# Performance work log

Measured on AMD Instinct MI355X. Metric: run time of the kernel, lower is better.

## Reference

```python
import jax, jax.numpy as jnp
import numpy as np

K = 4       # wavelet basis size
C = 4       # wavelet channels
ALPHA = 64  # retained Fourier modes per SparseKernelFT
L = 0       # coarsest-level cutoff


def setup_inputs() -> dict:
    key = jax.random.key(0)
    ks = jax.random.split(key, 14)
    B, N = 32, 16384
    ck = C * K
    wscale = 1.0 / (ck * ck)  # matches torch.rand(...)/in_ch^2 scale

    def cw(k1, k2):
        return (jax.random.normal(k1, (ck, ck, ALPHA), jnp.float32) * wscale,
                jax.random.normal(k2, (ck, ck, ALPHA), jnp.float32) * wscale)

    wA_re, wA_im = cw(ks[1], ks[2])
    wB_re, wB_im = cw(ks[3], ks[4])
    wC_re, wC_im = cw(ks[5], ks[6])
    fs = 1.0 / np.sqrt(2.0 * K)  # stand-in scale for orthonormal Legendre filter banks
    return {
        "x": jax.random.normal(ks[0], (B, N, C, K), jnp.float32),
        "ec_s": jax.random.normal(ks[7], (2 * K, K), jnp.float32) * fs,
        "ec_d": jax.random.normal(ks[8], (2 * K, K), jnp.float32) * fs,
        "rc_e": jax.random.normal(ks[9], (2 * K, K), jnp.float32) * fs,
        "rc_o": jax.random.normal(ks[10], (2 * K, K), jnp.float32) * fs,
        "t0_w": jax.random.normal(ks[11], (K, K), jnp.float32) / np.sqrt(K),
        "t0_b": jnp.zeros((K,), jnp.float32),
        "wA_re": wA_re, "wA_im": wA_im,
        "wB_re": wB_re, "wB_im": wB_im,
        "wC_re": wC_re, "wC_im": wC_im,
    }


def _sparse_ft(x, w_re, w_im):
    # SparseKernelFT (1D): rfft -> truncated-mode complex mixing -> irfft.
    B, N, c, k = x.shape
    ck = c * k
    xr = x.reshape(B, N, ck).transpose(0, 2, 1)        # (B, ck, N)
    xf = jnp.fft.rfft(xr)                               # (B, ck, N//2+1)
    nf = N // 2 + 1
    l = min(ALPHA, nf)
    w = (w_re + 1j * w_im)[:, :, :l]                    # (ck, ck, l) complex
    out = jnp.einsum('bix,iox->box', xf[:, :, :l], w)
    out_full = jnp.zeros((B, ck, nf), dtype=out.dtype).at[:, :, :l].set(out)
    y = jnp.fft.irfft(out_full, n=N)                    # real (B, ck, N)
    return y.transpose(0, 2, 1).reshape(B, N, c, k)


def _forward(x, ec_s, ec_d, rc_e, rc_o, t0_w, t0_b,
             wA_re, wA_im, wB_re, wB_im, wC_re, wC_im):
    B, N, c, k = x.shape
    ns = int(np.log2(N))
    Ud, Us = [], []
    # decomposition: N -> N/2 -> ... -> 2^L
    for _ in range(ns - L):
        xa = jnp.concatenate([x[:, ::2], x[:, 1::2]], axis=-1)  # (B, n/2, c, 2k)
        d = xa @ ec_d   # detail coefficients
        x = xa @ ec_s   # scale coefficients
        Ud.append(_sparse_ft(d, wA_re, wA_im) + _sparse_ft(x, wB_re, wB_im))
        Us.append(_sparse_ft(d, wC_re, wC_im))
    # coarsest-scale linear map T0 over last dim k
    x = x @ t0_w.T + t0_b
    # reconstruction with even/odd interleaving
    for i in range(ns - 1 - L, -1, -1):
        x = x + Us[i]
        xc = jnp.concatenate([x, Ud[i]], axis=-1)   # (B, n, c, 2k)
        x_e = xc @ rc_e                              # (B, n, c, k)
        x_o = xc @ rc_o
        b, n = x_e.shape[0], x_e.shape[1]
        x = jnp.stack([x_e, x_o], axis=2).reshape(b, 2 * n, c, k)
    return x


def reference(x, ec_s, ec_d, rc_e, rc_o, t0_w, t0_b,
              wA_re, wA_im, wB_re, wB_im, wC_re, wC_im):
    return _forward(x, ec_s, ec_d, rc_e, rc_o, t0_w, t0_b,
                    wA_re, wA_im, wB_re, wB_im, wC_re, wC_im)
```

## Files before the change

### kernel.cpp

```cpp
#include <hip/hip_runtime.h>

#define TWO_PI 6.28318530717958647692f

constexpr int BB   = 32;
constexpr int NTOT = 16384;
constexpr int CKd  = 16;
constexpr int NLEV = 14;

__device__ __forceinline__ void decomp_row(const float* __restrict__ src,
                                           const float* __restrict__ ec_s,
                                           const float* __restrict__ ec_d,
                                           float* d, float* s)
{
  float xa[32];
#pragma unroll
  for (int q = 0; q < 8; ++q) {
    float4 v = reinterpret_cast<const float4*>(src)[q];
    xa[q*4+0] = v.x; xa[q*4+1] = v.y; xa[q*4+2] = v.z; xa[q*4+3] = v.w;
  }
#pragma unroll
  for (int c = 0; c < 4; ++c) {
#pragma unroll
    for (int j = 0; j < 4; ++j) {
      float ad = 0.f, as = 0.f;
#pragma unroll
      for (int m = 0; m < 4; ++m) {
        const float xe = xa[c*4+m];
        const float xo = xa[16+c*4+m];
        ad += xe * ec_d[m*4+j] + xo * ec_d[(4+m)*4+j];
        as += xe * ec_s[m*4+j] + xo * ec_s[(4+m)*4+j];
      }
      d[c*4+j] = ad; s[c*4+j] = as;
    }
  }
}

__global__ __launch_bounds__(256) void fwd_big(
    const float* __restrict__ xin, float* __restrict__ xout,
    float* __restrict__ Fd, float* __restrict__ Fx,
    const float* __restrict__ ec_s, const float* __restrict__ ec_d,
    int nhalf)
{
  __shared__ float smem[16384];
  float* Pd = smem;
  float* Md = smem + 4096;
  float* Ps = smem + 8192;
  float* Ms = smem + 12288;
  const int b    = blockIdx.x;
  const int t0p  = blockIdx.y << 8;
  const int tid  = threadIdx.x;
  const int halfn = nhalf >> 1;
  const int p    = t0p + tid;

  float da[16], sa[16], db[16], sb[16];
  const size_t rowbase = (size_t)b * (2 * (size_t)nhalf) * CKd;
  decomp_row(xin + rowbase + (2*(size_t)p)*CKd,           ec_s, ec_d, da, sa);
  decomp_row(xin + rowbase + (2*(size_t)(p+halfn))*CKd,   ec_s, ec_d, db, sb);
  {
    float4* o0 = reinterpret_cast<float4*>(xout + ((size_t)b*nhalf + p)*CKd);
    float4* o1 = reinterpret_cast<float4*>(xout + ((size_t)b*nhalf + p + halfn)*CKd);
#pragma unroll
    for (int q = 0; q < 4; ++q) {
      o0[q] = make_float4(sa[q*4], sa[q*4+1], sa[q*4+2], sa[q*4+3]);
      o1[q] = make_float4(sb[q*4], sb[q*4+1], sb[q*4+2], sb[q*4+3]);
    }
  }
#pragma unroll
  for (int i = 0; i < 16; ++i) {
    Pd[tid*16+i] = da[i] + db[i];
    Md[tid*16+i] = da[i] - db[i];
    Ps[tid*16+i] = sa[i] + sb[i];
    Ms[tid*16+i] = sa[i] - sb[i];
  }
  __syncthreads();

  const int f = tid >> 2, g = tid & 3;
  const float* srcd = (f & 1) ? Md : Pd;
  const float* srcs = (f & 1) ? Ms : Ps;
  const int   mask = nhalf - 1;
  const float w    = TWO_PI / (float)nhalf;
  float cv, sv, c1, s1;
  __sincosf((float)((f * t0p) & mask) * w, &sv, &cv);
  __sincosf((float)f * w, &s1, &c1);
  float dre[4] = {0,0,0,0}, dim_[4] = {0,0,0,0};
  float sre[4] = {0,0,0,0}, sim_[4] = {0,0,0,0};
  for (int tt = 0; tt < 256; ++tt) {
    const float4 dv = *reinterpret_cast<const float4*>(srcd + tt*16 + g*4);
    const float4 xv = *reinterpret_cast<const float4*>(srcs + tt*16 + g*4);
    dre[0] += dv.x*cv; dim_[0] -= dv.x*sv;
    dre[1] += dv.y*cv; dim_[1] -= dv.y*sv;
    dre[2] += dv.z*cv; dim_[2] -= dv.z*sv;
    dre[3] += dv.w*cv; dim_[3] -= dv.w*sv;
    sre[0] += xv.x*cv; sim_[0] -= xv.x*sv;
    sre[1] += xv.y*cv; sim_[1] -= xv.y*sv;
    sre[2] += xv.z*cv; sim_[2] -= xv.z*sv;
    sre[3] += xv.w*cv; sim_[3] -= xv.w*sv;
    const float nc = cv*c1 - sv*s1;
    const float ns = sv*c1 + cv*s1;
    cv = nc; sv = ns;
  }
#pragma unroll
  for (int q = 0; q < 4; ++q) {
    const int i = g*4 + q;
    const int base = ((b * CKd + i) * 64 + f) * 2;
    atomicAdd(&Fd[base],   dre[q]);
    atomicAdd(&Fd[base+1], dim_[q]);
    atomicAdd(&Fx[base],   sre[q]);
    atomicAdd(&Fx[base+1], sim_[q]);
  }
}

__global__ __launch_bounds__(256) void mix2_kernel(
    float* __restrict__ Fd, float* __restrict__ Fx,
    float* __restrict__ G4,
    const float* __restrict__ wAre, const float* __restrict__ wAim,
    const float* __restrict__ wBre, const float* __restrict__ wBim,
    const float* __restrict__ wCre, const float* __restrict__ wCim)
{
  const int b  = blockIdx.x;
  const int tid = threadIdx.x;
  const int o  = tid >> 4;
  const int fs = tid & 15;

  const float4* Fd4 = reinterpret_cast<const float4*>(Fd);
  const float4* Fx4 = reinterpret_cast<const float4*>(Fx);

  float udre[4] = {0,0,0,0}, udim[4] = {0,0,0,0};
  float usre[4] = {0,0,0,0}, usim[4] = {0,0,0,0};

#pragma unroll 2
  for (int i = 0; i < 16; ++i) {
    const int wb4 = (i*16 + o)*16 + fs;
    const float4 war = reinterpret_cast<const float4*>(wAre)[wb4];
    const float4 wai = reinterpret_cast<const float4*>(wAim)[wb4];
    const float4 wbr = reinterpret_cast<const float4*>(wBre)[wb4];
    const float4 wbi = reinterpret_cast<const float4*>(wBim)[wb4];
    const float4 wcr = reinterpret_cast<const float4*>(wCre)[wb4];
    const float4 wci = reinterpret_cast<const float4*>(wCim)[wb4];
    const int fb4 = (b*16 + i)*32 + 2*fs;
    const float4 d01 = Fd4[fb4], d23 = Fd4[fb4+1];
    const float4 x01 = Fx4[fb4], x23 = Fx4[fb4+1];

    const float fdre[4] = {d01.x, d01.z, d23.x, d23.z};
    const float fdim[4] = {d01.y, d01.w, d23.y, d23.w};
    const float fxre[4] = {x01.x, x01.z, x23.x, x23.z};
    const float fxim[4] = {x01.y, x01.w, x23.y, x23.w};
    const float ware[4] = {war.x, war.y, war.z, war.w};
    const float waim[4] = {wai.x, wai.y, wai.z, wai.w};
    const float wbre[4] = {wbr.x, wbr.y, wbr.z, wbr.w};
    const float wbim[4] = {wbi.x, wbi.y, wbi.z, wbi.w};
    const float wcre[4] = {wcr.x, wcr.y, wcr.z, wcr.w};
    const float wcim[4] = {wci.x, wci.y, wci.z, wci.w};
#pragma unroll
    for (int j = 0; j < 4; ++j) {
      udre[j] += fdre[j]*ware[j] - fdim[j]*waim[j] + fxre[j]*wbre[j] - fxim[j]*wbim[j];
      udim[j] += fdre[j]*waim[j] + fdim[j]*ware[j] + fxre[j]*wbim[j] + fxim[j]*wbre[j];
      usre[j] += fdre[j]*wcre[j] - fdim[j]*wcim[j];
      usim[j] += fdre[j]*wcim[j] + fdim[j]*wcre[j];
    }
  }
  float4* G4f = reinterpret_cast<float4*>(G4);
#pragma unroll
  for (int j = 0; j < 4; ++j)
    G4f[(b*16 + o)*64 + 4*fs + j] = make_float4(udre[j], udim[j], usre[j], usim[j]);

  __syncthreads();
  {
    float4* Fdw = reinterpret_cast<float4*>(Fd);
    float4* Fxw = reinterpret_cast<float4*>(Fx);
    const int fb4 = (b*16 + o)*32 + 2*fs;
    const float4 z = make_float4(0.f, 0.f, 0.f, 0.f);
    Fdw[fb4] = z; Fdw[fb4+1] = z;
    Fxw[fb4] = z; Fxw[fb4+1] = z;
  }
}

__global__ __launch_bounds__(256) void inv_big(
    const float* __restrict__ G4, float* __restrict__ Ud, float* __restrict__ Us,
    int n)
{
  __shared__ float4 gl[64 * 17];
  const int b   = blockIdx.x;
  const int tid = threadIdx.x;
  const float4* Gb = reinterpret_cast<const float4*>(G4) + (size_t)b * 1024;
  for (int s_ = tid; s_ < 1024; s_ += 256) {
    const int i = s_ >> 6, f = s_ & 63;
    float4 v = Gb[(size_t)i * 64 + f];
    if (f) { v.x *= 2.f; v.y *= 2.f; v.z *= 2.f; v.w *= 2.f; }
    gl[f*17 + i] = v;
  }
  __syncthreads();

  const int i    = tid & 15;
  const int col  = tid >> 4;
  const int base = blockIdx.y << 7;
  const float w  = TWO_PI / (float)n;

  float udE[8], udO[8], usE[8], usO[8], c[8], s[8], c1[8], s1[8];
  {
    const float4 g0 = gl[i];
#pragma unroll
    for (int k = 0; k < 8; ++k) {
      udE[k] = g0.x; usE[k] = g0.z; udO[k] = 0.f; usO[k] = 0.f;
      __sincosf((float)(base + col + 16*k) * w, &s1[k], &c1[k]);
      c[k] = c1[k]; s[k] = s1[k];
    }
  }
  float4 ga = gl[17 + i];
#pragma unroll 1
  for (int kk = 0; kk < 31; ++kk) {
    const float4 gb = gl[(2*kk+2)*17 + i];
#pragma unroll
    for (int k = 0; k < 8; ++k) {
      udO[k] += ga.x*c[k] - ga.y*s[k];
      usO[k] += ga.z*c[k] - ga.w*s[k];
      const float nc = c[k]*c1[k] - s[k]*s1[k];
      const float ns = s[k]*c1[k] + c[k]*s1[k];
      c[k] = nc; s[k] = ns;
    }
    const float4 gn = gl[(2*kk+3)*17 + i];
#pragma unroll
    for (int k = 0; k < 8; ++k) {
      udE[k] += gb.x*c[k] - gb.y*s[k];
      usE[k] += gb.z*c[k] - gb.w*s[k];
      const float nc = c[k]*c1[k] - s[k]*s1[k];
      const float ns = s[k]*c1[k] + c[k]*s1[k];
      c[k] = nc; s[k] = ns;
    }
    ga = gn;
  }
#pragma unroll
  for (int k = 0; k < 8; ++k) {
    udO[k] += ga.x*c[k] - ga.y*s[k];
    usO[k] += ga.z*c[k] - ga.w*s[k];
  }
  const float invn = 1.f / (float)n;
  const int   half = n >> 1;
#pragma unroll
  for (int k = 0; k < 8; ++k) {
    const int t = base + col + 16*k;
    const size_t r0 = ((size_t)b*n + t) * CKd + i;
    const size_t r1 = r0 + (size_t)half * CKd;
    Ud[r0] = (udE[k] + udO[k]) * invn;
    Ud[r1] = (udE[k] - udO[k]) * invn;
    Us[r0] = (usE[k] + usO[k]) * invn;
    Us[r1] = (usE[k] - usO[k]) * invn;
  }
}

__global__ __launch_bounds__(256) void fwd_kernel(
    const float* __restrict__ xin, float* __restrict__ xout,
    float* __restrict__ Fd, float* __restrict__ Fx,
    const float* __restrict__ ec_s, const float* __restrict__ ec_d,
    int nhalf, int l)
{
  __shared__ float dt[256][20];
  __shared__ float st[256][20];
  const int b   = blockIdx.x;
  const int t0  = blockIdx.y << 8;
  const int tid = threadIdx.x;
  const int rem = nhalf - t0;
  const int rows = rem < 256 ? rem : 256;
  const int t = t0 + tid;

  if (tid < rows) {
    const float* src = xin + ((size_t)b * (2 * (size_t)nhalf) + 2 * (size_t)t) * CKd;
    float xa[32];
#pragma unroll
    for (int q = 0; q < 8; ++q) {
      float4 v = reinterpret_cast<const float4*>(src)[q];
      xa[q*4+0] = v.x; xa[q*4+1] = v.y; xa[q*4+2] = v.z; xa[q*4+3] = v.w;
    }
    float srow[16];
#pragma unroll
    for (int c = 0; c < 4; ++c) {
#pragma unroll
      for (int j = 0; j < 4; ++j) {
        float ad = 0.f, as = 0.f;
#pragma unroll
        for (int m = 0; m < 4; ++m) {
          const float xe = xa[c*4+m];
          const float xo = xa[16+c*4+m];
          ad += xe * ec_d[m*4+j] + xo * ec_d[(4+m)*4+j];
          as += xe * ec_s[m*4+j] + xo * ec_s[(4+m)*4+j];
        }
        dt[tid][c*4+j] = ad;
        st[tid][c*4+j] = as;
        srow[c*4+j]    = as;
      }
    }
    float4* dst = reinterpret_cast<float4*>(xout + ((size_t)b * nhalf + t) * CKd);
#pragma unroll
    for (int q = 0; q < 4; ++q)
      dst[q] = make_float4(srow[q*4], srow[q*4+1], srow[q*4+2], srow[q*4+3]);
  }
  __syncthreads();

  const int f = tid >> 2, g = tid & 3;
  if (f >= l) return;
  float dre[4] = {0,0,0,0}, dim_[4] = {0,0,0,0};
  float sre[4] = {0,0,0,0}, sim_[4] = {0,0,0,0};
  const int   mask = nhalf - 1;
  const float w    = TWO_PI / (float)nhalf;
  for (int tt = 0; tt < rows; ++tt) {
    const int tg = t0 + tt;
    float sv, cv;
    __sincosf((float)((f * tg) & mask) * w, &sv, &cv);
    const float4 dv = *reinterpret_cast<const float4*>(&dt[tt][g*4]);
    const float4 xv = *reinterpret_cast<const float4*>(&st[tt][g*4]);
    const float dvv[4] = {dv.x, dv.y, dv.z, dv.w};
    const float xvv[4] = {xv.x, xv.y, xv.z, xv.w};
#pragma unroll
    for (int q = 0; q < 4; ++q) {
      dre[q] += dvv[q] * cv;  dim_[q] -= dvv[q] * sv;
      sre[q] += xvv[q] * cv;  sim_[q] -= xvv[q] * sv;
    }
  }
#pragma unroll
  for (int q = 0; q < 4; ++q) {
    const int i = g*4 + q;
    const int base = ((b * CKd + i) * 64 + f) * 2;
    atomicAdd(&Fd[base],   dre[q]);
    atomicAdd(&Fd[base+1], dim_[q]);
    atomicAdd(&Fx[base],   sre[q]);
    atomicAdd(&Fx[base+1], sim_[q]);
  }
}

__global__ __launch_bounds__(256) void inv_kernel(
    const float* __restrict__ G4,
    float* __restrict__ Ud, float* __restrict__ Us, int n, int l)
{
  __shared__ float4 sG[64 * 16];
  const int b = blockIdx.x;
  const int tid = threadIdx.x;
  const float4* Gb = reinterpret_cast<const float4*>(G4) + (size_t)b * 1024;
  for (int s_ = tid; s_ < 1024; s_ += 256) {
    const int i = s_ >> 6, f = s_ & 63;
    if (f < l) sG[f*16 + i] = Gb[(size_t)i * 64 + f];
  }
  __syncthreads();
  const int t = (blockIdx.y << 8) + tid;
  if (t >= n) return;

  float ud[16], us[16];
#pragma unroll
  for (int i = 0; i < 16; ++i) { const float4 g = sG[i]; ud[i] = g.x; us[i] = g.z; }

  const int   mask = n - 1;
  const float w    = TWO_PI / (float)n;
  for (int f = 1; f < l; ++f) {
    float sv, cv;
    __sincosf((float)((f * t) & mask) * w, &sv, &cv);
    const float scale = (2 * f == n) ? 1.f : 2.f;
    cv *= scale; sv *= scale;
#pragma unroll
    for (int i = 0; i < 16; ++i) {
      const float4 g = sG[f * 16 + i];
      ud[i] += g.x * cv - g.y * sv;
      us[i] += g.z * cv - g.w * sv;
    }
  }
  const float invn = 1.f / (float)n;
  const size_t ro = ((size_t)b * n + t) * CKd;
  float4* pud = reinterpret_cast<float4*>(Ud + ro);
  float4* pus = reinterpret_cast<float4*>(Us + ro);
#pragma unroll
  for (int q = 0; q < 4; ++q) {
    pud[q] = make_float4(ud[q*4]*invn, ud[q*4+1]*invn, ud[q*4+2]*invn, ud[q*4+3]*invn);
    pus[q] = make_float4(us[q*4]*invn, us[q*4+1]*invn, us[q*4+2]*invn, us[q*4+3]*invn);
  }
}

__global__ void t0_kernel(const float* __restrict__ xin, float* __restrict__ xout,
                          const float* __restrict__ t0w, const float* __restrict__ t0b)
{
  const int idx = blockIdx.x * 256 + threadIdx.x;
  if (idx >= BB * CKd) return;
  const int bc = idx >> 2;
  const int k  = idx & 3;
  float acc = t0b[k];
#pragma unroll
  for (int j = 0; j < 4; ++j) acc += xin[bc*4 + j] * t0w[k*4 + j];
  xout[idx] = acc;
}

__global__ __launch_bounds__(256) void recon_kernel(
    const float* __restrict__ xin, const float* __restrict__ UsL,
    const float* __restrict__ UdL, float* __restrict__ xout,
    int n, int lg, const float* __restrict__ rc_e, const float* __restrict__ rc_o)
{
  const int idx = blockIdx.x * 256 + threadIdx.x;
  if (idx >= BB * n) return;
  const int b = idx >> lg;
  const int t = idx & (n - 1);
  const size_t ro = ((size_t)b * n + t) * CKd;
  float xv[16], uv[16], dv[16];
#pragma unroll
  for (int q = 0; q < 4; ++q) {
    const float4 a = reinterpret_cast<const float4*>(xin + ro)[q];
    const float4 u = reinterpret_cast<const float4*>(UsL + ro)[q];
    const float4 d = reinterpret_cast<const float4*>(UdL + ro)[q];
    xv[q*4]=a.x; xv[q*4+1]=a.y; xv[q*4+2]=a.z; xv[q*4+3]=a.w;
    uv[q*4]=u.x; uv[q*4+1]=u.y; uv[q*4+2]=u.z; uv[q*4+3]=u.w;
    dv[q*4]=d.x; dv[q*4+1]=d.y; dv[q*4+2]=d.z; dv[q*4+3]=d.w;
  }
  float xe[16], xo[16];
#pragma unroll
  for (int c = 0; c < 4; ++c) {
    float xc[8];
#pragma unroll
    for (int m = 0; m < 4; ++m) { xc[m] = xv[c*4+m] + uv[c*4+m]; xc[4+m] = dv[c*4+m]; }
#pragma unroll
    for (int k = 0; k < 4; ++k) {
      float ae = 0.f, ao = 0.f;
#pragma unroll
      for (int m = 0; m < 8; ++m) { ae += xc[m] * rc_e[m*4+k]; ao += xc[m] * rc_o[m*4+k]; }
      xe[c*4+k] = ae; xo[c*4+k] = ao;
    }
  }
  float4* out = reinterpret_cast<float4*>(xout + ((size_t)b * (2*(size_t)n) + 2*(size_t)t) * CKd);
#pragma unroll
  for (int q = 0; q < 4; ++q) {
    out[q]   = make_float4(xe[q*4], xe[q*4+1], xe[q*4+2], xe[q*4+3]);
    out[4+q] = make_float4(xo[q*4], xo[q*4+1], xo[q*4+2], xo[q*4+3]);
  }
}

extern "C" void kernel_launch(void* const* d_in, const int* in_sizes, int n_in,
                              void* d_out, int out_size, void* d_ws, size_t ws_size,
                              hipStream_t stream)
{
  const float* x    = (const float*)d_in[0];
  const float* ec_s = (const float*)d_in[1];
  const float* ec_d = (const float*)d_in[2];
  const float* rc_e = (const float*)d_in[3];
  const float* rc_o = (const float*)d_in[4];
  const float* t0w  = (const float*)d_in[5];
  const float* t0b  = (const float*)d_in[6];
  const float* wAre = (const float*)d_in[7];
  const float* wAim = (const float*)d_in[8];
  const float* wBre = (const float*)d_in[9];
  const float* wBim = (const float*)d_in[10];
  const float* wCre = (const float*)d_in[11];
  const float* wCim = (const float*)d_in[12];

  float* ws = (float*)d_ws;
  const size_t XS_ELEMS = (size_t)BB * (NTOT/2) * CKd;
  const size_t U_ELEMS  = (size_t)BB * (NTOT - 1) * CKd;
  const size_t F_ELEMS  = (size_t)BB * CKd * 64 * 2;
  float* xsA = ws;
  float* xsB = xsA + XS_ELEMS;
  float* UdS = xsB + XS_ELEMS;
  float* UsS = UdS + U_ELEMS;
  float* Fd  = UsS + U_ELEMS;
  float* Fx  = Fd + F_ELEMS;
  float* G4  = Fx + F_ELEMS;

  float* udl[NLEV]; float* usl[NLEV]; int nlv[NLEV];

  hipMemsetAsync(Fd, 0, 2 * F_ELEMS * sizeof(float), stream);

  const float* cur = x;
  float* nxt = xsA;
  size_t uoff = 0;
  int nhalf = NTOT / 2;
  for (int j = 0; j < NLEV; ++j, nhalf >>= 1) {
    const int l = (nhalf/2 + 1 < 64) ? (nhalf/2 + 1) : 64;
    udl[j] = UdS + uoff; usl[j] = UsS + uoff; nlv[j] = nhalf;
    if (nhalf >= 512) {
      fwd_big<<<dim3(BB, nhalf/512), 256, 0, stream>>>(cur, nxt, Fd, Fx, ec_s, ec_d, nhalf);
      mix2_kernel<<<BB, 256, 0, stream>>>(Fd, Fx, G4,
                                          wAre, wAim, wBre, wBim, wCre, wCim);
      inv_big<<<dim3(BB, nhalf/256), 256, 0, stream>>>(G4, udl[j], usl[j], nhalf);
    } else {
      fwd_kernel<<<dim3(BB, 1), 256, 0, stream>>>(cur, nxt, Fd, Fx, ec_s, ec_d, nhalf, l);
      mix2_kernel<<<BB, 256, 0, stream>>>(Fd, Fx, G4,
                                          wAre, wAim, wBre, wBim, wCre, wCim);
      inv_kernel<<<dim3(BB, 1), 256, 0, stream>>>(G4, udl[j], usl[j], nhalf, l);
    }
    uoff += (size_t)BB * nhalf * CKd;
    cur = nxt;
    nxt = (nxt == xsA) ? xsB : xsA;
  }

  t0_kernel<<<2, 256, 0, stream>>>(cur, nxt, t0w, t0b);
  cur = nxt;
  nxt = (nxt == xsA) ? xsB : xsA;

  for (int i = NLEV - 1; i >= 0; --i) {
    const int n = nlv[i];
    int lg = 0; while ((1 << lg) < n) ++lg;
    float* out = (i == 0) ? (float*)d_out : nxt;
    const int total = BB * n;
    recon_kernel<<<(total + 255) / 256, 256, 0, stream>>>(cur, usl[i], udl[i], out,
                                                          n, lg, rc_e, rc_o);
    cur = out;
    nxt = (nxt == xsA) ? xsB : xsA;
  }
}
```

Before: 712.6 us.

## Fuse small-level forward, mixing and inverse into one kernel; shrink big-level tiles

For levels with fewer than 512 half-points, the separate forward-DFT, mode-mixing and inverse kernels become one per-batch kernel. It keeps the Fourier coefficients in shared memory and uses rotation recurrences instead of per-element sincos, which removes atomics, global round trips and launches. The big-level forward kernel now has each thread decompose one row instead of two. It uses 128-row tiles with padded shared memory and an in-shared butterfly, doubling grid size and cutting shared memory use. The recurrence may add slight floating-point drift, and the big-level change doubles the atomic adds.

New measurement: 618.0 us. 1.15x faster.

```diff
diff --git a/kernel.cpp b/kernel.cpp
--- a/kernel.cpp
+++ b/kernel.cpp
@@ -41,52 +41,57 @@
     const float* __restrict__ ec_s, const float* __restrict__ ec_d,
     int nhalf)
 {
-  __shared__ float smem[16384];
+  __shared__ float smem[4 * 128 * 20];
   float* Pd = smem;
-  float* Md = smem + 4096;
-  float* Ps = smem + 8192;
-  float* Ms = smem + 12288;
+  float* Md = smem + 2560;
+  float* Ps = smem + 5120;
+  float* Ms = smem + 7680;
   const int b    = blockIdx.x;
-  const int t0p  = blockIdx.y << 8;
+  const int p0   = blockIdx.y << 7;
   const int tid  = threadIdx.x;
   const int halfn = nhalf >> 1;
-  const int p    = t0p + tid;
-
-  float da[16], sa[16], db[16], sb[16];
-  const size_t rowbase = (size_t)b * (2 * (size_t)nhalf) * CKd;
-  decomp_row(xin + rowbase + (2*(size_t)p)*CKd,           ec_s, ec_d, da, sa);
-  decomp_row(xin + rowbase + (2*(size_t)(p+halfn))*CKd,   ec_s, ec_d, db, sb);
+
   {
-    float4* o0 = reinterpret_cast<float4*>(xout + ((size_t)b*nhalf + p)*CKd);
-    float4* o1 = reinterpret_cast<float4*>(xout + ((size_t)b*nhalf + p + halfn)*CKd);
+    const int h = tid >> 7, r = tid & 127;
+    const int t = p0 + r + h * halfn;
+    float d[16], s[16];
+    const size_t rowbase = (size_t)b * (2 * (size_t)nhalf) * CKd;
+    decomp_row(xin + rowbase + (2*(size_t)t)*CKd, ec_s, ec_d, d, s);
+    float4* o0 = reinterpret_cast<float4*>(xout + ((size_t)b*nhalf + t)*CKd);
+    float* dd = (h ? Md : Pd) + r*20;
+    float* ds = (h ? Ms : Ps) + r*20;
 #pragma unroll
     for (int q = 0; q < 4; ++q) {
-      o0[q] = make_float4(sa[q*4], sa[q*4+1], sa[q*4+2], sa[q*4+3]);
-      o1[q] = make_float4(sb[q*4], sb[q*4+1], sb[q*4+2], sb[q*4+3]);
-    }
-  }
-#pragma unroll
-  for (int i = 0; i < 16; ++i) {
-    Pd[tid*16+i] = da[i] + db[i];
-    Md[tid*16+i] = da[i] - db[i];
-    Ps[tid*16+i] = sa[i] + sb[i];
-    Ms[tid*16+i] = sa[i] - sb[i];
-  }
-  __syncthreads();
-
-  const int f = tid >> 2, g = tid & 3;
+      o0[q] = make_float4(s[q*4], s[q*4+1], s[q*4+2], s[q*4+3]);
+      *reinterpret_cast<float4*>(dd + q*4) = make_float4(d[q*4], d[q*4+1], d[q*4+2], d[q*4+3]);
+      *reinterpret_cast<float4*>(ds + q*4) = make_float4(s[q*4], s[q*4+1], s[q*4+2], s[q*4+3]);
+    }
+  }
+  __syncthreads();
+#pragma unroll
+  for (int k = 0; k < 8; ++k) {
+    const int v = tid + (k << 8);
+    const int off = (v >> 4) * 20 + (v & 15);
+    const float a  = Pd[off], bb = Md[off];
+    Pd[off] = a + bb;  Md[off] = a - bb;
+    const float as = Ps[off], bs = Ms[off];
+    Ps[off] = as + bs; Ms[off] = as - bs;
+  }
+  __syncthreads();
+
+  const int g = tid >> 6, f = tid & 63;
   const float* srcd = (f & 1) ? Md : Pd;
   const float* srcs = (f & 1) ? Ms : Ps;
   const int   mask = nhalf - 1;
   const float w    = TWO_PI / (float)nhalf;
   float cv, sv, c1, s1;
-  __sincosf((float)((f * t0p) & mask) * w, &sv, &cv);
+  __sincosf((float)((f * p0) & mask) * w, &sv, &cv);
   __sincosf((float)f * w, &s1, &c1);
   float dre[4] = {0,0,0,0}, dim_[4] = {0,0,0,0};
   float sre[4] = {0,0,0,0}, sim_[4] = {0,0,0,0};
-  for (int tt = 0; tt < 256; ++tt) {
-    const float4 dv = *reinterpret_cast<const float4*>(srcd + tt*16 + g*4);
-    const float4 xv = *reinterpret_cast<const float4*>(srcs + tt*16 + g*4);
+  for (int tt = 0; tt < 128; ++tt) {
+    const float4 dv = *reinterpret_cast<const float4*>(srcd + tt*20 + g*4);
+    const float4 xv = *reinterpret_cast<const float4*>(srcs + tt*20 + g*4);
     dre[0] += dv.x*cv; dim_[0] -= dv.x*sv;
     dre[1] += dv.y*cv; dim_[1] -= dv.y*sv;
     dre[2] += dv.z*cv; dim_[2] -= dv.z*sv;
@@ -248,127 +253,126 @@
   }
 }
 
-__global__ __launch_bounds__(256) void fwd_kernel(
+__global__ __launch_bounds__(256) void small_level(
     const float* __restrict__ xin, float* __restrict__ xout,
-    float* __restrict__ Fd, float* __restrict__ Fx,
+    float* __restrict__ Ud, float* __restrict__ Us,
     const float* __restrict__ ec_s, const float* __restrict__ ec_d,
-    int nhalf, int l)
-{
-  __shared__ float dt[256][20];
-  __shared__ float st[256][20];
-  const int b   = blockIdx.x;
-  const int t0  = blockIdx.y << 8;
-  const int tid = threadIdx.x;
-  const int rem = nhalf - t0;
-  const int rows = rem < 256 ? rem : 256;
-  const int t = t0 + tid;
-
-  if (tid < rows) {
-    const float* src = xin + ((size_t)b * (2 * (size_t)nhalf) + 2 * (size_t)t) * CKd;
-    float xa[32];
-#pragma unroll
-    for (int q = 0; q < 8; ++q) {
-      float4 v = reinterpret_cast<const float4*>(src)[q];
-      xa[q*4+0] = v.x; xa[q*4+1] = v.y; xa[q*4+2] = v.z; xa[q*4+3] = v.w;
-    }
-    float srow[16];
-#pragma unroll
-    for (int c = 0; c < 4; ++c) {
-#pragma unroll
-      for (int j = 0; j < 4; ++j) {
-        float ad = 0.f, as = 0.f;
-#pragma unroll
-        for (int m = 0; m < 4; ++m) {
-          const float xe = xa[c*4+m];
-          const float xo = xa[16+c*4+m];
-          ad += xe * ec_d[m*4+j] + xo * ec_d[(4+m)*4+j];
-          as += xe * ec_s[m*4+j] + xo * ec_s[(4+m)*4+j];
+    const float* __restrict__ wAre, const float* __restrict__ wAim,
+    const float* __restrict__ wBre, const float* __restrict__ wBim,
+    const float* __restrict__ wCre, const float* __restrict__ wCim,
+    int nh, int l)
+{
+  __shared__ float smem[14592];
+  float*  dL = smem;
+  float*  sL = smem + 5120;
+  float4* F4 = reinterpret_cast<float4*>(smem + 10240);
+  float4* GL = reinterpret_cast<float4*>(smem);
+
+  const int b = blockIdx.x, tid = threadIdx.x;
+
+  if (tid < nh) {
+    float d[16], s[16];
+    decomp_row(xin + ((size_t)(b * 2 * nh + 2 * tid)) * CKd, ec_s, ec_d, d, s);
+    float* dd = dL + tid*20;
+    float* ds = sL + tid*20;
+    float4* o0 = reinterpret_cast<float4*>(xout + ((size_t)(b*nh + tid))*CKd);
+#pragma unroll
+    for (int q = 0; q < 4; ++q) {
+      *reinterpret_cast<float4*>(dd + q*4) = make_float4(d[q*4], d[q*4+1], d[q*4+2], d[q*4+3]);
+      *reinterpret_cast<float4*>(ds + q*4) = make_float4(s[q*4], s[q*4+1], s[q*4+2], s[q*4+3]);
+      o0[q] = make_float4(s[q*4], s[q*4+1], s[q*4+2], s[q*4+3]);
+    }
+  }
+  __syncthreads();
+
+  {
+    const int g = tid >> 6, f = tid & 63;
+    if (f < l) {
+      const float w = TWO_PI / (float)nh;
+      float cv = 1.f, sv = 0.f, c1, s1;
+      __sincosf((float)f * w, &s1, &c1);
+      float dre[4] = {0,0,0,0}, dim_[4] = {0,0,0,0};
+      float sre[4] = {0,0,0,0}, sim_[4] = {0,0,0,0};
+      for (int tt = 0; tt < nh; ++tt) {
+        const float4 dv = *reinterpret_cast<const float4*>(dL + tt*20 + g*4);
+        const float4 xv = *reinterpret_cast<const float4*>(sL + tt*20 + g*4);
+        dre[0] += dv.x*cv; dim_[0] -= dv.x*sv;
+        dre[1] += dv.y*cv; dim_[1] -= dv.y*sv;
+        dre[2] += dv.z*cv; dim_[2] -= dv.z*sv;
+        dre[3] += dv.w*cv; dim_[3] -= dv.w*sv;
+        sre[0] += xv.x*cv; sim_[0] -= xv.x*sv;
+        sre[1] += xv.y*cv; sim_[1] -= xv.y*sv;
+        sre[2] += xv.z*cv; sim_[2] -= xv.z*sv;
+        sre[3] += xv.w*cv; sim_[3] -= xv.w*sv;
+        const float nc = cv*c1 - sv*s1;
+        const float ns = sv*c1 + cv*s1;
+        cv = nc; sv = ns;
+      }
+#pragma unroll
+      for (int q = 0; q < 4; ++q)
+        F4[f*17 + g*4 + q] = make_float4(dre[q], dim_[q], sre[q], sim_[q]);
+    }
+  }
+  __syncthreads();
+
+  {
+    const int o2 = tid >> 6, f = tid & 63;
+    if (f < l) {
+      float udre[4] = {0,0,0,0}, udim[4] = {0,0,0,0};
+      float usre[4] = {0,0,0,0}, usim[4] = {0,0,0,0};
+#pragma unroll 4
+      for (int i = 0; i < 16; ++i) {
+        const float4 Fv = F4[f*17 + i];
+#pragma unroll
+        for (int q = 0; q < 4; ++q) {
+          const int o  = o2*4 + q;
+          const int wb = (i * CKd + o) * 64 + f;
+          const float war = wAre[wb], wai = wAim[wb];
+          const float wbr = wBre[wb], wbi = wBim[wb];
+          const float wcr = wCre[wb], wci = wCim[wb];
+          udre[q] += Fv.x*war - Fv.y*wai + Fv.z*wbr - Fv.w*wbi;
+          udim[q] += Fv.x*wai + Fv.y*war + Fv.z*wbi + Fv.w*wbr;
+          usre[q] += Fv.x*wcr - Fv.y*wci;
+          usim[q] += Fv.x*wci + Fv.y*wcr;
         }
-        dt[tid][c*4+j] = ad;
-        st[tid][c*4+j] = as;
-        srow[c*4+j]    = as;
       }
-    }
-    float4* dst = reinterpret_cast<float4*>(xout + ((size_t)b * nhalf + t) * CKd);
-#pragma unroll
-    for (int q = 0; q < 4; ++q)
-      dst[q] = make_float4(srow[q*4], srow[q*4+1], srow[q*4+2], srow[q*4+3]);
-  }
-  __syncthreads();
-
-  const int f = tid >> 2, g = tid & 3;
-  if (f >= l) return;
-  float dre[4] = {0,0,0,0}, dim_[4] = {0,0,0,0};
-  float sre[4] = {0,0,0,0}, sim_[4] = {0,0,0,0};
-  const int   mask = nhalf - 1;
-  const float w    = TWO_PI / (float)nhalf;
-  for (int tt = 0; tt < rows; ++tt) {
-    const int tg = t0 + tt;
-    float sv, cv;
-    __sincosf((float)((f * tg) & mask) * w, &sv, &cv);
-    const float4 dv = *reinterpret_cast<const float4*>(&dt[tt][g*4]);
-    const float4 xv = *reinterpret_cast<const float4*>(&st[tt][g*4]);
-    const float dvv[4] = {dv.x, dv.y, dv.z, dv.w};
-    const float xvv[4] = {xv.x, xv.y, xv.z, xv.w};
+#pragma unroll
+      for (int q = 0; q < 4; ++q)
+        GL[f*17 + o2*4 + q] = make_float4(udre[q], udim[q], usre[q], usim[q]);
+    }
+  }
+  __syncthreads();
+
+  if (tid < nh) {
+    const int t = tid;
+    const float w = TWO_PI / (float)nh;
+    float ud[16], us[16];
+#pragma unroll
+    for (int i = 0; i < 16; ++i) { const float4 g = GL[i]; ud[i] = g.x; us[i] = g.z; }
+    float c1, s1;
+    __sincosf((float)t * w, &s1, &c1);
+    float cv = c1, sv = s1;
+    for (int f = 1; f < l; ++f) {
+      const float scale = (2*f == nh) ? 1.f : 2.f;
+      const float c2 = cv * scale, s2 = sv * scale;
+#pragma unroll
+      for (int i = 0; i < 16; ++i) {
+        const float4 g = GL[f*17 + i];
+        ud[i] += g.x*c2 - g.y*s2;
+        us[i] += g.z*c2 - g.w*s2;
+      }
+      const float nc = cv*c1 - sv*s1, ns = sv*c1 + cv*s1;
+      cv = nc; sv = ns;
+    }
+    const float invn = 1.f / (float)nh;
+    const size_t ro = ((size_t)(b*nh + t)) * CKd;
+    float4* pu = reinterpret_cast<float4*>(Ud + ro);
+    float4* pv = reinterpret_cast<float4*>(Us + ro);
 #pragma unroll
     for (int q = 0; q < 4; ++q) {
-      dre[q] += dvv[q] * cv;  dim_[q] -= dvv[q] * sv;
-      sre[q] += xvv[q] * cv;  sim_[q] -= xvv[q] * sv;
-    }
-  }
-#pragma unroll
-  for (int q = 0; q < 4; ++q) {
-    const int i = g*4 + q;
-    const int base = ((b * CKd + i) * 64 + f) * 2;
-    atomicAdd(&Fd[base],   dre[q]);
-    atomicAdd(&Fd[base+1], dim_[q]);
-    atomicAdd(&Fx[base],   sre[q]);
-    atomicAdd(&Fx[base+1], sim_[q]);
-  }
-}
-
-__global__ __launch_bounds__(256) void inv_kernel(
-    const float* __restrict__ G4,
-    float* __restrict__ Ud, float* __restrict__ Us, int n, int l)
-{
-  __shared__ float4 sG[64 * 16];
-  const int b = blockIdx.x;
-  const int tid = threadIdx.x;
-  const float4* Gb = reinterpret_cast<const float4*>(G4) + (size_t)b * 1024;
-  for (int s_ = tid; s_ < 1024; s_ += 256) {
-    const int i = s_ >> 6, f = s_ & 63;
-    if (f < l) sG[f*16 + i] = Gb[(size_t)i * 64 + f];
-  }
-  __syncthreads();
-  const int t = (blockIdx.y << 8) + tid;
-  if (t >= n) return;
-
-  float ud[16], us[16];
-#pragma unroll
-  for (int i = 0; i < 16; ++i) { const float4 g = sG[i]; ud[i] = g.x; us[i] = g.z; }
-
-  const int   mask = n - 1;
-  const float w    = TWO_PI / (float)n;
-  for (int f = 1; f < l; ++f) {
-    float sv, cv;
-    __sincosf((float)((f * t) & mask) * w, &sv, &cv);
-    const float scale = (2 * f == n) ? 1.f : 2.f;
-    cv *= scale; sv *= scale;
-#pragma unroll
-    for (int i = 0; i < 16; ++i) {
-      const float4 g = sG[f * 16 + i];
-      ud[i] += g.x * cv - g.y * sv;
-      us[i] += g.z * cv - g.w * sv;
-    }
-  }
-  const float invn = 1.f / (float)n;
-  const size_t ro = ((size_t)b * n + t) * CKd;
-  float4* pud = reinterpret_cast<float4*>(Ud + ro);
-  float4* pus = reinterpret_cast<float4*>(Us + ro);
-#pragma unroll
-  for (int q = 0; q < 4; ++q) {
-    pud[q] = make_float4(ud[q*4]*invn, ud[q*4+1]*invn, ud[q*4+2]*invn, ud[q*4+3]*invn);
-    pus[q] = make_float4(us[q*4]*invn, us[q*4+1]*invn, us[q*4+2]*invn, us[q*4+3]*invn);
+      pu[q] = make_float4(ud[q*4]*invn, ud[q*4+1]*invn, ud[q*4+2]*invn, ud[q*4+3]*invn);
+      pv[q] = make_float4(us[q*4]*invn, us[q*4+1]*invn, us[q*4+2]*invn, us[q*4+3]*invn);
+    }
   }
 }
 
@@ -469,15 +473,14 @@
     const int l = (nhalf/2 + 1 < 64) ? (nhalf/2 + 1) : 64;
     udl[j] = UdS + uoff; usl[j] = UsS + uoff; nlv[j] = nhalf;
     if (nhalf >= 512) {
-      fwd_big<<<dim3(BB, nhalf/512), 256, 0, stream>>>(cur, nxt, Fd, Fx, ec_s, ec_d, nhalf);
+      fwd_big<<<dim3(BB, nhalf/256), 256, 0, stream>>>(cur, nxt, Fd, Fx, ec_s, ec_d, nhalf);
       mix2_kernel<<<BB, 256, 0, stream>>>(Fd, Fx, G4,
                                           wAre, wAim, wBre, wBim, wCre, wCim);
       inv_big<<<dim3(BB, nhalf/256), 256, 0, stream>>>(G4, udl[j], usl[j], nhalf);
     } else {
-      fwd_kernel<<<dim3(BB, 1), 256, 0, stream>>>(cur, nxt, Fd, Fx, ec_s, ec_d, nhalf, l);
-      mix2_kernel<<<BB, 256, 0, stream>>>(Fd, Fx, G4,
-                                          wAre, wAim, wBre, wBim, wCre, wCim);
-      inv_kernel<<<dim3(BB, 1), 256, 0, stream>>>(G4, udl[j], usl[j], nhalf, l);
+      small_level<<<BB, 256, 0, stream>>>(cur, nxt, udl[j], usl[j], ec_s, ec_d,
+                                          wAre, wAim, wBre, wBim, wCre, wCim,
+                                          nhalf, l);
     }
     uoff += (size_t)BB * nhalf * CKd;
     cur = nxt;
```
